# Kernel tuning notes

Hardware: AMD Instinct MI355X
Metric: run time of the kernel (lower is better)

Reference implementation:

```python
import jax, jax.numpy as jnp
import numpy as np

N, D, R = 65536, 32, 128


def setup_inputs() -> dict:
    key = jax.random.key(0)
    k1, k2, k3, k4 = jax.random.split(key, 4)
    X = jax.random.normal(k1, (N, D), dtype=jnp.float32)
    a = jax.random.normal(k2, (R, D), dtype=jnp.float32)
    b = jax.random.uniform(k3, (R, D), dtype=jnp.float32)  # positive, like abs(randn)
    c = jax.random.normal(k4, (R, D + 1), dtype=jnp.float32)
    return {"X": X, "a": a, "b": b, "c": c}


def reference(X, a, b, c):
    # Gaussian membership per (sample, rule, dim): exp(-(x-a)^2 / (2*clamp(b,1e-8)^2))
    b_cl = jnp.clip(b, 1e-8)                      # [R, D]
    diff = X[:, None, :] - a[None, :, :]          # [N, R, D]
    mu = jnp.exp(-(diff * diff) / (2.0 * b_cl * b_cl))
    strengths = jnp.prod(mu, axis=2)              # [N, R] rule firing strengths
    strengths_sum = jnp.sum(strengths, axis=1, keepdims=True)
    normalized = strengths / (strengths_sum + 1e-8)
    # consequent: linear model per rule, X @ c[:, :-1].T + bias
    rule_out = X @ c[:, :-1].T + c[:, -1]         # [N, R]
    predictions = jnp.sum(normalized * rule_out, axis=1)  # [N]
    return (predictions, strengths, normalized)
```

## Files before the change

kernel.cpp:

```cpp
#include <hip/hip_runtime.h>

#define NS 65536
#define DD 32
#define RR 128
#define SPB 32
#define STR 132
#define NBLK (NS / SPB)

typedef float f2 __attribute__((ext_vector_type(2)));

static __device__ __forceinline__ f2 pkfma(f2 a, f2 b, f2 c) {
    f2 d;
    asm("v_pk_fma_f32 %0, %1, %2, %3" : "=v"(d) : "v"(a), "v"(b), "v"(c));
    return d;
}

static __device__ __forceinline__ float dpp_x1(float x) {
    return __int_as_float(__builtin_amdgcn_update_dpp(
        0, __float_as_int(x), 0xB1 , 0xF, 0xF, true));
}

__global__ __launch_bounds__(256, 4) void anfis_main(
    const float* __restrict__ X, const float* __restrict__ A,
    const float* __restrict__ B, const float* __restrict__ C,
    float* __restrict__ out_pred, float* __restrict__ out_str,
    float* __restrict__ out_norm)
{
    __shared__ float SBUF[SPB * STR];
    __shared__ float PBUF[SPB * STR];
    __shared__ float XT[SPB * DD];
    __shared__ float pS[SPB][8];
    __shared__ float pD[SPB][8];
    __shared__ float scale_lds[SPB];

    const int tid   = threadIdx.x;
    const int rule  = tid >> 1;
    const int half  = tid & 1;
    const int xoff  = half * 16;
    const int nbase = blockIdx.x * SPB;

    ((float4*)XT)[tid] = ((const float4*)(X + (size_t)nbase * DD))[tid];

    f2 w01_[4], w23_[4], n01_[4], n23_[4], c01_[4], c23_[4];
    float biasv;
    {
        const float4* av = (const float4*)(A + rule * DD + xoff);
        const float4* bv = (const float4*)(B + rule * DD + xoff);
        const float*  cp = C + rule * (DD + 1) + xoff;
        #pragma unroll
        for (int i = 0; i < 4; ++i) {
            float4 va = av[i], vb = bv[i];
            float w0 = 0.8493218003f * __builtin_amdgcn_rcpf(fmaxf(vb.x, 1e-8f));
            float w1 = 0.8493218003f * __builtin_amdgcn_rcpf(fmaxf(vb.y, 1e-8f));
            float w2 = 0.8493218003f * __builtin_amdgcn_rcpf(fmaxf(vb.z, 1e-8f));
            float w3 = 0.8493218003f * __builtin_amdgcn_rcpf(fmaxf(vb.w, 1e-8f));
            w01_[i] = f2{w0, w1};            w23_[i] = f2{w2, w3};
            n01_[i] = f2{-va.x * w0, -va.y * w1};
            n23_[i] = f2{-va.z * w2, -va.w * w3};
            c01_[i] = f2{cp[4*i + 0], cp[4*i + 1]};
            c23_[i] = f2{cp[4*i + 2], cp[4*i + 3]};
        }
        biasv = half ? C[rule * (DD + 1) + DD] : 0.0f;
    }
    __syncthreads();

    #pragma unroll
    for (int i = 0; i < 4; ++i)
        asm("" : "+v"(w01_[i]), "+v"(w23_[i]), "+v"(n01_[i]),
                 "+v"(n23_[i]), "+v"(c01_[i]), "+v"(c23_[i]));
    asm("" : "+v"(biasv));

    float* wbuf = half ? PBUF : SBUF;

    #define LOADQ(buf, jj) { _Pragma("unroll") \
        for (int g = 0; g < 4; ++g) \
            buf[g] = *(const float4*)&XT[(jj) * DD + xoff + g * 4]; }

    #define DOSAMPLE(buf, jj) { \
        f2 s01 = f2{0.f, 0.f}, s23 = f2{0.f, 0.f}; \
        f2 r01 = f2{biasv, 0.f}, r23 = f2{0.f, 0.f}; \
        _Pragma("unroll") \
        for (int g = 0; g < 4; ++g) { \
            const f2* xp2 = (const f2*)&buf[g]; \
            f2 x01 = xp2[0], x23 = xp2[1]; \
            f2 t01 = pkfma(x01, w01_[g], n01_[g]); \
            s01 = pkfma(t01, t01, s01); \
            r01 = pkfma(x01, c01_[g], r01); \
            f2 t23 = pkfma(x23, w23_[g], n23_[g]); \
            s23 = pkfma(t23, t23, s23); \
            r23 = pkfma(x23, c23_[g], r23); \
        } \
        float sh = (s01.x + s01.y) + (s23.x + s23.y); \
        float rh = (r01.x + r01.y) + (r23.x + r23.y); \
        float stot = sh + dpp_x1(sh); \
        float rtot = rh + dpp_x1(rh); \
        float st = __builtin_amdgcn_exp2f(-stot); \
        wbuf[(jj) * STR + rule] = half ? st * rtot : st; }

    float4 qa[4], qb[4];
    LOADQ(qa, 0)
    for (int j = 0; j < SPB; j += 2) {
        LOADQ(qb, j + 1)
        DOSAMPLE(qa, j)
        if (j + 2 < SPB) LOADQ(qa, j + 2)
        DOSAMPLE(qb, j + 1)
    }
    #undef LOADQ
    #undef DOSAMPLE
    __syncthreads();

    {
        int s = tid >> 3, o = tid & 7;
        const float4* srow = (const float4*)&SBUF[s * STR + o * 16];
        const float4* prow = (const float4*)&PBUF[s * STR + o * 16];
        float ss = 0.f, dd = 0.f;
        #pragma unroll
        for (int k = 0; k < 4; ++k) {
            float4 v = srow[k]; ss += (v.x + v.y) + (v.z + v.w);
            float4 p = prow[k]; dd += (p.x + p.y) + (p.z + p.w);
        }
        pS[s][o] = ss; pD[s][o] = dd;
    }
    __syncthreads();
    float predv = 0.f;
    if (tid < SPB) {
        float ss = 0.f, dd = 0.f;
        #pragma unroll
        for (int o = 0; o < 8; ++o) { ss += pS[tid][o]; dd += pD[tid][o]; }
        float sc = 1.0f / (ss + 1e-8f);
        predv = dd * sc;
        scale_lds[tid] = sc;
    }
    __syncthreads();
    if (tid < SPB) out_pred[nbase + tid] = predv;

    #pragma unroll
    for (int it = 0; it < 4; ++it) {
        int f   = it * 256 + tid;
        int row = f >> 5;
        int col = f & 31;
        float4 v = *(const float4*)&SBUF[row * STR + col * 4];
        float sc = scale_lds[row];
        size_t base = ((size_t)(nbase + row)) * RR + col * 4;
        *(float4*)(out_str  + base) = v;
        *(float4*)(out_norm + base) = make_float4(v.x * sc, v.y * sc, v.z * sc, v.w * sc);
    }
}

extern "C" void kernel_launch(void* const* d_in, const int* in_sizes, int n_in,
                              void* d_out, int out_size, void* d_ws, size_t ws_size,
                              hipStream_t stream) {
    const float* X = (const float*)d_in[0];
    const float* A = (const float*)d_in[1];
    const float* B = (const float*)d_in[2];
    const float* C = (const float*)d_in[3];

    float* pred = (float*)d_out;
    float* str  = pred + NS;
    float* nrm  = str + (size_t)NS * RR;

    anfis_main<<<dim3(NBLK), dim3(256), 0, stream>>>(X, A, B, C, pred, str, nrm);
}
```

Before: 100.3 us.

## Split each rule across four lanes with 512-thread blocks

```diff
diff --git a/kernel.cpp b/kernel.cpp
--- a/kernel.cpp
+++ b/kernel.cpp
@@ -14,13 +14,21 @@
     asm("v_pk_fma_f32 %0, %1, %2, %3" : "=v"(d) : "v"(a), "v"(b), "v"(c));
     return d;
 }
-
+static __device__ __forceinline__ f2 pkadd(f2 a, f2 b) {
+    f2 d;
+    asm("v_pk_add_f32 %0, %1, %2" : "=v"(d) : "v"(a), "v"(b));
+    return d;
+}
 static __device__ __forceinline__ float dpp_x1(float x) {
     return __int_as_float(__builtin_amdgcn_update_dpp(
         0, __float_as_int(x), 0xB1 , 0xF, 0xF, true));
 }
+static __device__ __forceinline__ float dpp_x2(float x) {
+    return __int_as_float(__builtin_amdgcn_update_dpp(
+        0, __float_as_int(x), 0x4E , 0xF, 0xF, true));
+}
 
-__global__ __launch_bounds__(256, 4) void anfis_main(
+__global__ __launch_bounds__(512, 6) void anfis_main(
     const float* __restrict__ X, const float* __restrict__ A,
     const float* __restrict__ B, const float* __restrict__ C,
     float* __restrict__ out_pred, float* __restrict__ out_str,
@@ -34,70 +42,63 @@
     __shared__ float scale_lds[SPB];
 
     const int tid   = threadIdx.x;
-    const int rule  = tid >> 1;
-    const int half  = tid & 1;
-    const int xoff  = half * 16;
+    const int rule  = tid >> 2;
+    const int q     = tid & 3;
     const int nbase = blockIdx.x * SPB;
 
-    ((float4*)XT)[tid] = ((const float4*)(X + (size_t)nbase * DD))[tid];
+    if (tid < 256)
+        ((float4*)XT)[tid] = ((const float4*)(X + (size_t)nbase * DD))[tid];
 
-    f2 w01_[4], w23_[4], n01_[4], n23_[4], c01_[4], c23_[4];
+    f2 w_[4], n_[4], c_[4];
     float biasv;
     {
-        const float4* av = (const float4*)(A + rule * DD + xoff);
-        const float4* bv = (const float4*)(B + rule * DD + xoff);
-        const float*  cp = C + rule * (DD + 1) + xoff;
+        const float4* av = (const float4*)(A + rule * DD + q * 8);
+        const float4* bv = (const float4*)(B + rule * DD + q * 8);
+        const float*  cp = C + rule * (DD + 1) + q * 8;
         #pragma unroll
-        for (int i = 0; i < 4; ++i) {
+        for (int i = 0; i < 2; ++i) {
             float4 va = av[i], vb = bv[i];
             float w0 = 0.8493218003f * __builtin_amdgcn_rcpf(fmaxf(vb.x, 1e-8f));
             float w1 = 0.8493218003f * __builtin_amdgcn_rcpf(fmaxf(vb.y, 1e-8f));
             float w2 = 0.8493218003f * __builtin_amdgcn_rcpf(fmaxf(vb.z, 1e-8f));
             float w3 = 0.8493218003f * __builtin_amdgcn_rcpf(fmaxf(vb.w, 1e-8f));
-            w01_[i] = f2{w0, w1};            w23_[i] = f2{w2, w3};
-            n01_[i] = f2{-va.x * w0, -va.y * w1};
-            n23_[i] = f2{-va.z * w2, -va.w * w3};
-            c01_[i] = f2{cp[4*i + 0], cp[4*i + 1]};
-            c23_[i] = f2{cp[4*i + 2], cp[4*i + 3]};
+            w_[2*i+0] = f2{w0, w1};          w_[2*i+1] = f2{w2, w3};
+            n_[2*i+0] = f2{-va.x * w0, -va.y * w1};
+            n_[2*i+1] = f2{-va.z * w2, -va.w * w3};
+            c_[2*i+0] = f2{cp[4*i + 0], cp[4*i + 1]};
+            c_[2*i+1] = f2{cp[4*i + 2], cp[4*i + 3]};
         }
-        biasv = half ? C[rule * (DD + 1) + DD] : 0.0f;
+        biasv = (q == 3) ? C[rule * (DD + 1) + DD] : 0.0f;
     }
     __syncthreads();
 
     #pragma unroll
     for (int i = 0; i < 4; ++i)
-        asm("" : "+v"(w01_[i]), "+v"(w23_[i]), "+v"(n01_[i]),
-                 "+v"(n23_[i]), "+v"(c01_[i]), "+v"(c23_[i]));
+        asm("" : "+v"(w_[i]), "+v"(n_[i]), "+v"(c_[i]));
     asm("" : "+v"(biasv));
 
-    float* wbuf = half ? PBUF : SBUF;
+    float* wbuf = (q & 1) ? PBUF : SBUF;
 
-    #define LOADQ(buf, jj) { _Pragma("unroll") \
-        for (int g = 0; g < 4; ++g) \
-            buf[g] = *(const float4*)&XT[(jj) * DD + xoff + g * 4]; }
+    #define LOADQ(buf, jj) { \
+        buf[0] = *(const float4*)&XT[(jj) * DD + q * 8]; \
+        buf[1] = *(const float4*)&XT[(jj) * DD + q * 8 + 4]; }
 
     #define DOSAMPLE(buf, jj) { \
-        f2 s01 = f2{0.f, 0.f}, s23 = f2{0.f, 0.f}; \
-        f2 r01 = f2{biasv, 0.f}, r23 = f2{0.f, 0.f}; \
+        f2 s = f2{0.f, 0.f}, r = f2{biasv, 0.f}; \
+        const f2* xp = (const f2*)buf; \
         _Pragma("unroll") \
         for (int g = 0; g < 4; ++g) { \
-            const f2* xp2 = (const f2*)&buf[g]; \
-            f2 x01 = xp2[0], x23 = xp2[1]; \
-            f2 t01 = pkfma(x01, w01_[g], n01_[g]); \
-            s01 = pkfma(t01, t01, s01); \
-            r01 = pkfma(x01, c01_[g], r01); \
-            f2 t23 = pkfma(x23, w23_[g], n23_[g]); \
-            s23 = pkfma(t23, t23, s23); \
-            r23 = pkfma(x23, c23_[g], r23); \
+            f2 t = pkfma(xp[g], w_[g], n_[g]); \
+            s = pkfma(t, t, s); \
+            r = pkfma(xp[g], c_[g], r); \
         } \
-        float sh = (s01.x + s01.y) + (s23.x + s23.y); \
-        float rh = (r01.x + r01.y) + (r23.x + r23.y); \
-        float stot = sh + dpp_x1(sh); \
-        float rtot = rh + dpp_x1(rh); \
-        float st = __builtin_amdgcn_exp2f(-stot); \
-        wbuf[(jj) * STR + rule] = half ? st * rtot : st; }
+        f2 v = f2{s.x + s.y, r.x + r.y}; \
+        v = pkadd(v, f2{dpp_x1(v.x), dpp_x1(v.y)}); \
+        v = pkadd(v, f2{dpp_x2(v.x), dpp_x2(v.y)}); \
+        float st = __builtin_amdgcn_exp2f(-v.x); \
+        if (q < 2) wbuf[(jj) * STR + rule] = q ? st * v.y : st; }
 
-    float4 qa[4], qb[4];
+    float4 qa[2], qb[2];
     LOADQ(qa, 0)
     for (int j = 0; j < SPB; j += 2) {
         LOADQ(qb, j + 1)
@@ -109,7 +110,7 @@
     #undef DOSAMPLE
     __syncthreads();
 
-    {
+    if (tid < 256) {
         int s = tid >> 3, o = tid & 7;
         const float4* srow = (const float4*)&SBUF[s * STR + o * 16];
         const float4* prow = (const float4*)&PBUF[s * STR + o * 16];
@@ -135,8 +136,8 @@
     if (tid < SPB) out_pred[nbase + tid] = predv;
 
     #pragma unroll
-    for (int it = 0; it < 4; ++it) {
-        int f   = it * 256 + tid;
+    for (int it = 0; it < 2; ++it) {
+        int f   = it * 512 + tid;
         int row = f >> 5;
         int col = f & 31;
         float4 v = *(const float4*)&SBUF[row * STR + col * 4];
@@ -159,5 +160,5 @@
     float* str  = pred + NS;
     float* nrm  = str + (size_t)NS * RR;
 
-    anfis_main<<<dim3(NBLK), dim3(256), 0, stream>>>(X, A, B, C, pred, str, nrm);
+    anfis_main<<<dim3(NBLK), dim3(512), 0, stream>>>(X, A, B, C, pred, str, nrm);
 }
```

Result: slower. 104.6 us (+4.3%).
